# Performance work log

Measured on AMD Instinct MI355X. Metric: run time of the kernel, lower is better.

## Reference

```python
import jax, jax.numpy as jnp
import numpy as np
import math

B, T, EMB = 2, 2048, 2048
HQ = HKV = 16
HD = EMB // HQ  # 128
MAX_SEQ = 2048


def _rope(x, cos, sin):
    # x: [b, t, h, d]; pairs are consecutive (view_as_complex on reshape(..., -1, 2))
    b, t, h, d = x.shape
    xp = x.astype(jnp.float32).reshape(b, t, h, d // 2, 2)
    xr, xi = xp[..., 0], xp[..., 1]
    c = cos[None, :, None, :]  # [1, t, 1, d/2]
    s = sin[None, :, None, :]
    or_ = xr * c - xi * s
    oi_ = xr * s + xi * c
    out = jnp.stack([or_, oi_], axis=-1).reshape(b, t, h, d)
    return out.astype(x.dtype)


def setup_inputs() -> dict:
    key = jax.random.key(0)
    ks = jax.random.split(key, 6)
    x = jax.random.normal(ks[0], (B, T, EMB), dtype=jnp.float32)
    # torch Linear weights: [out_features, in_features], y = x @ W.T
    sc = 1.0 / math.sqrt(EMB)
    wq = jax.random.normal(ks[1], (EMB, EMB), dtype=jnp.float32) * sc
    wk = jax.random.normal(ks[2], (EMB, EMB), dtype=jnp.float32) * sc
    wv = jax.random.normal(ks[3], (EMB, EMB), dtype=jnp.float32) * sc
    wo = jax.random.normal(ks[4], (EMB, EMB), dtype=jnp.float32) * sc
    # RoPE frequencies (llama-style), head_dim/2 angles per position
    inv_freq = 1.0 / (10000.0 ** (np.arange(0, HD, 2, dtype=np.float32) / HD))
    angles = np.arange(T, dtype=np.float32)[:, None] * inv_freq[None, :]  # [T, HD/2]
    freqs_cos = jnp.asarray(np.cos(angles))
    freqs_sin = jnp.asarray(np.sin(angles))
    k_cache = jnp.zeros((B, MAX_SEQ, HKV, HD), dtype=jnp.float32)
    v_cache = jnp.zeros((B, MAX_SEQ, HKV, HD), dtype=jnp.float32)
    return {"x": x, "wq": wq, "wk": wk, "wv": wv, "wo": wo,
            "k_cache": k_cache, "v_cache": v_cache,
            "freqs_cos": freqs_cos, "freqs_sin": freqs_sin, "start_pos": 0}


def reference(x, wq, wk, wv, wo, k_cache, v_cache, freqs_cos, freqs_sin, start_pos):
    b, t, c = x.shape
    xq = (x @ wq.T).reshape(b, t, HQ, HD)
    xk = (x @ wk.T).reshape(b, t, HKV, HD)
    xv = (x @ wv.T).reshape(b, t, HKV, HD)
    xq = _rope(xq, freqs_cos, freqs_sin)
    xk = _rope(xk, freqs_cos, freqs_sin)
    # KV-cache update at start_pos, then read prefix [0, start_pos+t)
    k_cache = jax.lax.dynamic_update_slice(k_cache, xk, (0, start_pos, 0, 0))
    v_cache = jax.lax.dynamic_update_slice(v_cache, xv, (0, start_pos, 0, 0))
    keys = k_cache[:, :start_pos + t]    # [b, s, hkv, d]
    values = v_cache[:, :start_pos + t]
    # n_rep = HQ // HKV = 1 -> repeat_kv is identity
    q = xq.transpose(0, 2, 1, 3)         # [b, h, t, d]
    k = keys.transpose(0, 2, 1, 3)       # [b, h, s, d]
    v = values.transpose(0, 2, 1, 3)
    scores = jnp.einsum('bhtd,bhsd->bhts', q, k) / math.sqrt(HD)
    scores = jax.nn.softmax(scores.astype(jnp.float32), axis=-1).astype(q.dtype)
    out = jnp.einsum('bhts,bhsd->bhtd', scores, v)
    out = out.transpose(0, 2, 1, 3).reshape(b, t, -1)
    return out @ wo.T
```

## Files before the change

kernel.cpp:

```cpp
#include <hip/hip_runtime.h>
#include <cstdint>

using u16 = unsigned short;
using short8 = __attribute__((ext_vector_type(8))) short;
using floatx4 = __attribute__((ext_vector_type(4))) float;

__device__ __forceinline__ u16 f2b(float f) {
    unsigned u = __float_as_uint(f);
    u = (u + 0x7fffu + ((u >> 16) & 1u)) >> 16;
    return (u16)u;
}
__device__ __forceinline__ u16 f2b_fast(float f) {
    return (u16)((__float_as_uint(f) + 0x8000u) >> 16);
}
__device__ __forceinline__ float b2f(unsigned v) {
    return __uint_as_float(v << 16);
}
__device__ __forceinline__ float fast_exp2(float f) {
#if __has_builtin(__builtin_amdgcn_exp2f)
    return __builtin_amdgcn_exp2f(f);
#else
    return exp2f(f);
#endif
}
__device__ __forceinline__ void gl_lds16(const u16* g, u16* l) {
    __builtin_amdgcn_global_load_lds(
        (const __attribute__((address_space(1))) void*)(const void*)g,
        (__attribute__((address_space(3))) void*)(void*)l, 16, 0, 0);
}

__global__ void cvt5_kernel(const float* __restrict__ x, const float* __restrict__ wq,
                            const float* __restrict__ wk, const float* __restrict__ wv,
                            const float* __restrict__ wo, u16* __restrict__ xb,
                            u16* __restrict__ wqkvb, u16* __restrict__ wob) {
    int i = blockIdx.x * 256 + threadIdx.x;
    const float* src;
    u16* dst;
    int off;
    if (i < 2097152)      { src = x;  dst = xb;             off = i; }
    else if (i < 3145728) { src = wq; dst = wqkvb;          off = i - 2097152; }
    else if (i < 4194304) { src = wk; dst = wqkvb + 4194304; off = i - 3145728; }
    else if (i < 5242880) { src = wv; dst = wqkvb + 8388608; off = i - 4194304; }
    else                  { src = wo; dst = wob;            off = i - 5242880; }
    float4 v = ((const float4*)src)[off];
    uint2 o;
    o.x = (unsigned)f2b(v.x) | ((unsigned)f2b(v.y) << 16);
    o.y = (unsigned)f2b(v.z) | ((unsigned)f2b(v.w) << 16);
    *(uint2*)&dst[off * 4] = o;
}

template <int OUT_F32, int DO_ROPE>
__global__ void gemm_bt(const u16* __restrict__ A, const u16* __restrict__ B,
                        void* __restrict__ Cp, const float* __restrict__ fc,
                        const float* __restrict__ fs, int M, int N, int K) {
    __shared__ u16 As[128 * 64];
    __shared__ u16 Bs[128 * 64];
    const int tid = threadIdx.x;
    const int lane = tid & 63, w = tid >> 6;
    const int wm = w & 1, wn = w >> 1;
    const int m0 = blockIdx.y * 128, n0 = blockIdx.x * 128;
    const int r = lane & 15, q = lane >> 4;

    floatx4 acc[4][4] = {};

    for (int k0 = 0; k0 < K; k0 += 64) {
        __syncthreads();
#pragma unroll
        for (int i = 0; i < 4; i++) {
            int c = i * 256 + tid;
            int row = c >> 3, slot = c & 7;
            int sch = (slot ^ (row & 7)) * 8;
            gl_lds16(A + (size_t)(m0 + row) * K + k0 + sch, As + c * 8);
            gl_lds16(B + (size_t)(n0 + row) * K + k0 + sch, Bs + c * 8);
        }
        __syncthreads();
#pragma unroll
        for (int ks = 0; ks < 2; ks++) {
            const int sw = ((ks * 4 + q) ^ (r & 7)) * 8;
            short8 af[4], bf[4];
#pragma unroll
            for (int mi = 0; mi < 4; mi++)
                af[mi] = *(const short8*)&As[(wm * 64 + mi * 16 + r) * 64 + sw];
#pragma unroll
            for (int ni = 0; ni < 4; ni++)
                bf[ni] = *(const short8*)&Bs[(wn * 64 + ni * 16 + r) * 64 + sw];
#pragma unroll
            for (int mi = 0; mi < 4; mi++)
#pragma unroll
                for (int ni = 0; ni < 4; ni++)
                    acc[mi][ni] = __builtin_amdgcn_mfma_f32_16x16x32_bf16(af[mi], bf[ni], acc[mi][ni], 0, 0, 0);
        }
    }
    const bool rope = DO_ROPE && (n0 < 4096);
#pragma unroll
    for (int mi = 0; mi < 4; mi++)
#pragma unroll
        for (int ni = 0; ni < 4; ni++)
#pragma unroll
            for (int rr = 0; rr < 4; rr++) {
                int row = m0 + wm * 64 + mi * 16 + q * 4 + rr;
                int col = n0 + wn * 64 + ni * 16 + r;
                float val = acc[mi][ni][rr];
                if (rope) {
                    int t = row & 2047;
                    int d2 = (col & 127) >> 1;
                    float cv = fc[t * 64 + d2], sv = fs[t * 64 + d2];
                    float partner = __shfl_xor(val, 1);
                    val = (r & 1) ? (partner * sv + val * cv)
                                  : (val * cv - partner * sv);
                }
                if (OUT_F32)
                    ((float*)Cp)[(size_t)row * N + col] = val;
                else
                    ((u16*)Cp)[(size_t)row * N + col] = f2b(val);
            }
}

__global__ void vtrans_kernel(const u16* __restrict__ xqkv, u16* __restrict__ vt) {
    __shared__ u16 Ts[64][72];
    int bh = blockIdx.z, d0 = blockIdx.y * 64, t0 = blockIdx.x * 64;
    int b = bh >> 4, h = bh & 15;
#pragma unroll
    for (int i = 0; i < 2; i++) {
        int c = i * 256 + threadIdx.x;
        int tr = c >> 3, c8 = (c & 7) * 8;
        short8 v = *(const short8*)&xqkv[(size_t)(b * 2048 + t0 + tr) * 6144 + 4096 + h * 128 + d0 + c8];
#pragma unroll
        for (int j = 0; j < 8; j++) Ts[tr][c8 + j] = ((u16)v[j]);
    }
    __syncthreads();
#pragma unroll
    for (int i = 0; i < 2; i++) {
        int c = i * 256 + threadIdx.x;
        int dr = c >> 3, t8 = (c & 7) * 8;
        short8 v;
#pragma unroll
        for (int j = 0; j < 8; j++) v[j] = (short)Ts[t8 + j][dr];
        *(short8*)&vt[((size_t)(bh * 128 + d0 + dr)) * 2048 + t0 + t8] = v;
    }
}

__global__ __launch_bounds__(256, 2) void flash_kernel(const u16* __restrict__ xqkv,
                                                       const u16* __restrict__ vt,
                                                       u16* __restrict__ ao) {
    __shared__ u16 smem[25600];
    u16* Ks = smem;
    u16* Vs = smem + 8192;
    const int tid = threadIdx.x;
    const int lane = tid & 63, w = tid >> 6;
    const int qg = lane >> 4, r16 = lane & 15;
    const int swz = (qg ^ ((r16 >> 1) & 3)) * 8;
    u16* QPw = smem + 16384 + w * 2304;
    const int bh = blockIdx.y, b = bh >> 4, h = bh & 15;
    const int t0 = blockIdx.x * 128 + w * 32;
    const float sl2e = 0.08838834764831845f * 1.4426950408889634f;

    short8 qreg[2][4];
#pragma unroll
    for (int tf = 0; tf < 2; tf++)
#pragma unroll
        for (int kc = 0; kc < 4; kc++) {
            short8 qv = *(const short8*)&xqkv[(size_t)(b * 2048 + t0 + tf * 16 + r16) * 6144 +
                                              h * 128 + kc * 32 + qg * 8];
#pragma unroll
            for (int j = 0; j < 8; j++)
                qv[j] = (short)f2b(b2f((u16)qv[j]) * sl2e);
            qreg[tf][kc] = qv;
        }

    floatx4 oacc[2][8] = {};
    float lsum[2][4] = {};

    for (int s0 = 0; s0 < 2048; s0 += 64) {
        __syncthreads();
#pragma unroll
        for (int i = 0; i < 4; i++) {
            int c = i * 256 + tid;
            int kc = c >> 8, cc = c & 255, sr = cc >> 2, slot = cc & 3;
            int sch = (slot ^ ((sr >> 1) & 3)) * 8;
            gl_lds16(xqkv + (size_t)(b * 2048 + s0 + sr) * 6144 + 2048 + h * 128 + kc * 32 + sch,
                     Ks + c * 8);
        }
#pragma unroll
        for (int i = 0; i < 4; i++) {
            int c = i * 256 + tid;
            int sc = c >> 9, cc = c & 511, d = cc >> 2, slot = cc & 3;
            int sch = (slot ^ ((d >> 1) & 3)) * 8;
            gl_lds16(vt + (size_t)(bh * 128 + d) * 2048 + s0 + sc * 32 + sch, Vs + c * 8);
        }
        __syncthreads();

        floatx4 sacc[2][4] = {};
#pragma unroll
        for (int kc = 0; kc < 4; kc++)
#pragma unroll
            for (int ni = 0; ni < 4; ni++) {
                short8 bfr = *(const short8*)&Ks[kc * 2048 + (ni * 16 + r16) * 32 + swz];
                sacc[0][ni] = __builtin_amdgcn_mfma_f32_16x16x32_bf16(qreg[0][kc], bfr, sacc[0][ni], 0, 0, 0);
                sacc[1][ni] = __builtin_amdgcn_mfma_f32_16x16x32_bf16(qreg[1][kc], bfr, sacc[1][ni], 0, 0, 0);
            }

#pragma unroll
        for (int tf = 0; tf < 2; tf++)
#pragma unroll
            for (int ni = 0; ni < 4; ni++)
#pragma unroll
                for (int r = 0; r < 4; r++) {
                    float p = fast_exp2(sacc[tf][ni][r]);
                    lsum[tf][r] += p;
                    QPw[(tf * 16 + qg * 4 + r) * 72 + ni * 16 + r16] = f2b_fast(p);
                }

#pragma unroll
        for (int sc = 0; sc < 2; sc++) {
            short8 p0 = *(const short8*)&QPw[(r16) * 72 + sc * 32 + qg * 8];
            short8 p1 = *(const short8*)&QPw[(16 + r16) * 72 + sc * 32 + qg * 8];
#pragma unroll
            for (int dt = 0; dt < 8; dt++) {
                short8 a = *(const short8*)&Vs[sc * 4096 + (dt * 16 + r16) * 32 + swz];
                oacc[0][dt] = __builtin_amdgcn_mfma_f32_16x16x32_bf16(a, p0, oacc[0][dt], 0, 0, 0);
                oacc[1][dt] = __builtin_amdgcn_mfma_f32_16x16x32_bf16(a, p1, oacc[1][dt], 0, 0, 0);
            }
        }
    }

#pragma unroll
    for (int mm = 1; mm <= 8; mm <<= 1)
#pragma unroll
        for (int tf = 0; tf < 2; tf++)
#pragma unroll
            for (int r = 0; r < 4; r++) lsum[tf][r] += __shfl_xor(lsum[tf][r], mm);

    int src = (r16 >> 2) << 4;
#pragma unroll
    for (int tf = 0; tf < 2; tf++) {
        float l0 = __shfl(lsum[tf][0], src), l1 = __shfl(lsum[tf][1], src);
        float l2 = __shfl(lsum[tf][2], src), l3 = __shfl(lsum[tf][3], src);
        float lsel = (r16 & 2) ? ((r16 & 1) ? l3 : l2) : ((r16 & 1) ? l1 : l0);
        float inv = 1.0f / lsel;
#pragma unroll
        for (int dt = 0; dt < 8; dt++)
#pragma unroll
            for (int r = 0; r < 4; r++)
                QPw[r16 * 136 + dt * 16 + qg * 4 + r] = f2b(oacc[tf][dt][r] * inv);
#pragma unroll
        for (int i = 0; i < 4; i++) {
            int c = i * 64 + lane;
            int rowt = c >> 4, c8 = (c & 15) * 8;
            short8 v = *(const short8*)&QPw[rowt * 136 + c8];
            *(short8*)&ao[(size_t)(b * 2048 + t0 + tf * 16 + rowt) * 2048 + h * 128 + c8] = v;
        }
    }
}

extern "C" void kernel_launch(void* const* d_in, const int* in_sizes, int n_in,
                              void* d_out, int out_size, void* d_ws, size_t ws_size,
                              hipStream_t stream) {
    const float* x = (const float*)d_in[0];
    const float* wq = (const float*)d_in[1];
    const float* wk = (const float*)d_in[2];
    const float* wv = (const float*)d_in[3];
    const float* wo = (const float*)d_in[4];
    const float* fcos = (const float*)d_in[7];
    const float* fsin = (const float*)d_in[8];

    char* ws = (char*)d_ws;
    u16* xb    = (u16*)(ws);
    u16* wqkvb = (u16*)(ws + 16777216);
    u16* wob   = (u16*)(ws + 41943040);
    u16* xqkv  = (u16*)(ws + 50331648);
    u16* vt    = (u16*)(ws + 100663296);
    u16* ao    = (u16*)(ws + 117440512);

    cvt5_kernel<<<24576, 256, 0, stream>>>(x, wq, wk, wv, wo, xb, wqkvb, wob);
    gemm_bt<0, 1><<<dim3(48, 32), 256, 0, stream>>>(xb, wqkvb, xqkv, fcos, fsin, 4096, 6144, 2048);
    vtrans_kernel<<<dim3(32, 2, 32), 256, 0, stream>>>(xqkv, vt);
    flash_kernel<<<dim3(16, 32), 256, 0, stream>>>(xqkv, vt, ao);
    gemm_bt<1, 0><<<dim3(16, 32), 256, 0, stream>>>(ao, wob, (float*)d_out, nullptr, nullptr, 4096, 2048, 2048);
}
```

Baseline: 443.6 us.

## Replace QKV projection GEMM with 256x256 tiled, double-buffered, ping-pong MFMA kernel

Adds a new gemm256 kernel for the fused QKV projection. It uses 256x256 tiles with 512 threads, asynchronous global-to-LDS loads double-buffered across K tiles, swizzled LDS reads and 16x16x32 bf16 MFMA with setprio to interleave memory and compute. The goal is more operand reuse per load and better latency hiding than the 128x128 gemm_bt. RoPE stays fused in the epilogue. The cost is high register pressure, 64KB of LDS per block, and only 384 blocks, which may leave some CUs unevenly loaded.

```diff
diff --git a/kernel.cpp b/kernel.cpp
--- a/kernel.cpp
+++ b/kernel.cpp
@@ -28,6 +28,13 @@
         (const __attribute__((address_space(1))) void*)(const void*)g,
         (__attribute__((address_space(3))) void*)(void*)l, 16, 0, 0);
 }
+
+#define BARF()                                  \
+    do {                                        \
+        asm volatile("" ::: "memory");          \
+        __builtin_amdgcn_s_barrier();           \
+        asm volatile("" ::: "memory");          \
+    } while (0)
 
 __global__ void cvt5_kernel(const float* __restrict__ x, const float* __restrict__ wq,
                             const float* __restrict__ wk, const float* __restrict__ wv,
@@ -49,6 +56,119 @@
     *(uint2*)&dst[off * 4] = o;
 }
 
+#define MFMA16(MH)                                                             \
+    __builtin_amdgcn_s_setprio(1);                                             \
+    _Pragma("unroll") for (int i_ = 0; i_ < 4; i_++) {                         \
+        _Pragma("unroll") for (int n_ = 0; n_ < 4; n_++)                       \
+            acc[(MH) * 4 + i_][n_] = __builtin_amdgcn_mfma_f32_16x16x32_bf16(  \
+                af[i_], bf[n_], acc[(MH) * 4 + i_][n_], 0, 0, 0);              \
+    }                                                                          \
+    __builtin_amdgcn_s_setprio(0);
+
+template <int DO_ROPE>
+__global__ __launch_bounds__(512, 2) void gemm256(const u16* __restrict__ A,
+                                                  const u16* __restrict__ B,
+                                                  u16* __restrict__ C,
+                                                  const float* __restrict__ fc,
+                                                  const float* __restrict__ fs,
+                                                  int M, int N, int K) {
+    __shared__ u16 lds[2][2][2][8192];
+    const int tid = threadIdx.x;
+    const int lane = tid & 63, w = tid >> 6;
+    const int wm = w >> 2, wn = w & 3;
+    const int m0 = blockIdx.y * 256, n0 = blockIdx.x * 256;
+    const int r16 = lane & 15, qg = lane >> 4;
+    const int swz8 = (qg ^ ((r16 >> 1) & 3)) * 8;
+    const int nt = K >> 6;
+
+    const int sr = tid >> 2;
+    const int sc0 = ((tid & 3) ^ ((sr >> 1) & 3)) * 8;
+    const size_t offA0 = (size_t)(m0 + sr) * K + sc0;
+    const size_t offB0 = (size_t)(n0 + sr) * K + sc0;
+    const size_t off1 = (size_t)128 * K;
+
+    auto stage = [&](int mat, int ks, int tile) {
+        const u16* s = (mat ? B + offB0 : A + offA0) + tile * 64 + ks * 32;
+        u16* d = &lds[tile & 1][mat][ks][tid * 8];
+        gl_lds16(s, d);
+        gl_lds16(s + off1, d + 4096);
+    };
+
+    floatx4 acc[8][4] = {};
+
+    stage(0, 0, 0); stage(1, 0, 0); stage(0, 1, 0); stage(1, 1, 0);
+    stage(0, 0, 1); stage(1, 0, 1); stage(0, 1, 1);
+    asm volatile("s_waitcnt vmcnt(6)" ::: "memory");
+    BARF();
+
+    const int abase = (wm * 128 + r16) * 32 + swz8;
+    const int bbase = (wn * 64 + r16) * 32 + swz8;
+
+    for (int t = 0; t < nt; ++t) {
+        const int buf = t & 1;
+        const u16* LA0 = &lds[buf][0][0][0];
+        const u16* LA1 = &lds[buf][0][1][0];
+        const u16* LB0 = &lds[buf][1][0][0];
+        const u16* LB1 = &lds[buf][1][1][0];
+        short8 af[4], bf[4];
+
+#pragma unroll
+        for (int n_ = 0; n_ < 4; n_++) bf[n_] = *(const short8*)&LB0[bbase + n_ * 512];
+#pragma unroll
+        for (int i_ = 0; i_ < 4; i_++) af[i_] = *(const short8*)&LA0[abase + i_ * 512];
+        if (t + 1 < nt) stage(1, 1, t + 1);
+        BARF();
+        MFMA16(0)
+        BARF();
+
+#pragma unroll
+        for (int i_ = 0; i_ < 4; i_++) af[i_] = *(const short8*)&LA0[abase + 2048 + i_ * 512];
+        BARF();
+        MFMA16(1)
+        if (t + 2 < nt) stage(0, 0, t + 2);
+        BARF();
+
+#pragma unroll
+        for (int n_ = 0; n_ < 4; n_++) bf[n_] = *(const short8*)&LB1[bbase + n_ * 512];
+#pragma unroll
+        for (int i_ = 0; i_ < 4; i_++) af[i_] = *(const short8*)&LA1[abase + i_ * 512];
+        if (t + 2 < nt) stage(1, 0, t + 2);
+        BARF();
+        MFMA16(0)
+        BARF();
+
+#pragma unroll
+        for (int i_ = 0; i_ < 4; i_++) af[i_] = *(const short8*)&LA1[abase + 2048 + i_ * 512];
+        BARF();
+        MFMA16(1)
+        if (t + 2 < nt) stage(0, 1, t + 2);
+        if (t + 2 < nt)      asm volatile("s_waitcnt vmcnt(6)" ::: "memory");
+        else if (t + 1 < nt) asm volatile("s_waitcnt vmcnt(0)" ::: "memory");
+        BARF();
+    }
+
+    const bool rope = DO_ROPE && (n0 < 4096);
+#pragma unroll
+    for (int mi = 0; mi < 8; mi++)
+#pragma unroll
+        for (int ni = 0; ni < 4; ni++)
+#pragma unroll
+            for (int rr = 0; rr < 4; rr++) {
+                int row = m0 + wm * 128 + mi * 16 + qg * 4 + rr;
+                int col = n0 + wn * 64 + ni * 16 + r16;
+                float val = acc[mi][ni][rr];
+                if (rope) {
+                    int tt = row & 2047;
+                    int d2 = (col & 127) >> 1;
+                    float cv = fc[tt * 64 + d2], sv = fs[tt * 64 + d2];
+                    float partner = __shfl_xor(val, 1);
+                    val = (r16 & 1) ? (partner * sv + val * cv)
+                                    : (val * cv - partner * sv);
+                }
+                C[(size_t)row * N + col] = f2b(val);
+            }
+}
+
 template <int OUT_F32, int DO_ROPE>
 __global__ void gemm_bt(const u16* __restrict__ A, const u16* __restrict__ B,
                         void* __restrict__ Cp, const float* __restrict__ fc,
@@ -273,7 +393,7 @@
     u16* ao    = (u16*)(ws + 117440512);
 
     cvt5_kernel<<<24576, 256, 0, stream>>>(x, wq, wk, wv, wo, xb, wqkvb, wob);
-    gemm_bt<0, 1><<<dim3(48, 32), 256, 0, stream>>>(xb, wqkvb, xqkv, fcos, fsin, 4096, 6144, 2048);
+    gemm256<1><<<dim3(24, 16), 512, 0, stream>>>(xb, wqkvb, xqkv, fcos, fsin, 4096, 6144, 2048);
     vtrans_kernel<<<dim3(32, 2, 32), 256, 0, stream>>>(xqkv, vt);
     flash_kernel<<<dim3(16, 32), 256, 0, stream>>>(xqkv, vt, ao);
     gemm_bt<1, 0><<<dim3(16, 32), 256, 0, stream>>>(ao, wob, (float*)d_out, nullptr, nullptr, 4096, 2048, 2048);
```

Result: slower. 476.0 us (+7.3%).

## Read K/V fragments directly from global memory in flash kernel, drop LDS staging

Applied to the files above, without the earlier changes.

The flash attention kernel no longer stages K and V tiles into shared memory with barriers. Each wave now loads its MFMA B/A fragments straight from global memory, relying on L2/cache reuse across the four waves and across blocks. The grid is swapped so consecutive blocks share the same head, which improves cache locality for K/V. This removes the per-tile syncthreads and LDS traffic but turns each fragment read into a strided global load with higher latency and four-fold redundant traffic per block.

```diff
diff --git a/kernel.cpp b/kernel.cpp
--- a/kernel.cpp
+++ b/kernel.cpp
@@ -143,16 +143,13 @@
 __global__ __launch_bounds__(256, 2) void flash_kernel(const u16* __restrict__ xqkv,
                                                        const u16* __restrict__ vt,
                                                        u16* __restrict__ ao) {
-    __shared__ u16 smem[25600];
-    u16* Ks = smem;
-    u16* Vs = smem + 8192;
+    __shared__ u16 QP[4 * 2304];
     const int tid = threadIdx.x;
     const int lane = tid & 63, w = tid >> 6;
     const int qg = lane >> 4, r16 = lane & 15;
-    const int swz = (qg ^ ((r16 >> 1) & 3)) * 8;
-    u16* QPw = smem + 16384 + w * 2304;
-    const int bh = blockIdx.y, b = bh >> 4, h = bh & 15;
-    const int t0 = blockIdx.x * 128 + w * 32;
+    u16* QPw = QP + w * 2304;
+    const int bh = blockIdx.x, b = bh >> 4, h = bh & 15;
+    const int t0 = blockIdx.y * 128 + w * 32;
     const float sl2e = 0.08838834764831845f * 1.4426950408889634f;
 
     short8 qreg[2][4];
@@ -171,31 +168,19 @@
     floatx4 oacc[2][8] = {};
     float lsum[2][4] = {};
 
+    const u16* Kg0 = xqkv + (size_t)(b * 2048) * 6144 + 2048 + h * 128;
+    const u16* Vg0 = vt + (size_t)(bh * 128) * 2048;
+
     for (int s0 = 0; s0 < 2048; s0 += 64) {
-        __syncthreads();
-#pragma unroll
-        for (int i = 0; i < 4; i++) {
-            int c = i * 256 + tid;
-            int kc = c >> 8, cc = c & 255, sr = cc >> 2, slot = cc & 3;
-            int sch = (slot ^ ((sr >> 1) & 3)) * 8;
-            gl_lds16(xqkv + (size_t)(b * 2048 + s0 + sr) * 6144 + 2048 + h * 128 + kc * 32 + sch,
-                     Ks + c * 8);
-        }
-#pragma unroll
-        for (int i = 0; i < 4; i++) {
-            int c = i * 256 + tid;
-            int sc = c >> 9, cc = c & 511, d = cc >> 2, slot = cc & 3;
-            int sch = (slot ^ ((d >> 1) & 3)) * 8;
-            gl_lds16(vt + (size_t)(bh * 128 + d) * 2048 + s0 + sc * 32 + sch, Vs + c * 8);
-        }
-        __syncthreads();
+        const u16* Kg = Kg0 + (size_t)s0 * 6144;
+        const u16* Vg = Vg0 + s0;
 
         floatx4 sacc[2][4] = {};
 #pragma unroll
         for (int kc = 0; kc < 4; kc++)
 #pragma unroll
             for (int ni = 0; ni < 4; ni++) {
-                short8 bfr = *(const short8*)&Ks[kc * 2048 + (ni * 16 + r16) * 32 + swz];
+                short8 bfr = *(const short8*)&Kg[(size_t)(ni * 16 + r16) * 6144 + kc * 32 + qg * 8];
                 sacc[0][ni] = __builtin_amdgcn_mfma_f32_16x16x32_bf16(qreg[0][kc], bfr, sacc[0][ni], 0, 0, 0);
                 sacc[1][ni] = __builtin_amdgcn_mfma_f32_16x16x32_bf16(qreg[1][kc], bfr, sacc[1][ni], 0, 0, 0);
             }
@@ -217,7 +202,7 @@
             short8 p1 = *(const short8*)&QPw[(16 + r16) * 72 + sc * 32 + qg * 8];
 #pragma unroll
             for (int dt = 0; dt < 8; dt++) {
-                short8 a = *(const short8*)&Vs[sc * 4096 + (dt * 16 + r16) * 32 + swz];
+                short8 a = *(const short8*)&Vg[(size_t)(dt * 16 + r16) * 2048 + sc * 32 + qg * 8];
                 oacc[0][dt] = __builtin_amdgcn_mfma_f32_16x16x32_bf16(a, p0, oacc[0][dt], 0, 0, 0);
                 oacc[1][dt] = __builtin_amdgcn_mfma_f32_16x16x32_bf16(a, p1, oacc[1][dt], 0, 0, 0);
             }
@@ -275,6 +260,6 @@
     cvt5_kernel<<<24576, 256, 0, stream>>>(x, wq, wk, wv, wo, xb, wqkvb, wob);
     gemm_bt<0, 1><<<dim3(48, 32), 256, 0, stream>>>(xb, wqkvb, xqkv, fcos, fsin, 4096, 6144, 2048);
     vtrans_kernel<<<dim3(32, 2, 32), 256, 0, stream>>>(xqkv, vt);
-    flash_kernel<<<dim3(16, 32), 256, 0, stream>>>(xqkv, vt, ao);
+    flash_kernel<<<dim3(32, 16), 256, 0, stream>>>(xqkv, vt, ao);
     gemm_bt<1, 0><<<dim3(16, 32), 256, 0, stream>>>(ao, wob, (float*)d_out, nullptr, nullptr, 4096, 2048, 2048);
 }
```

Measured after the change: 557.7 us. 25.7% more time.

## Double-buffer K tiles and split V load wait in flash attention

Applied to the files above, without the earlier changes.

Restructures the flash attention loop so the next K tile is prefetched into a second LDS buffer while the current tile is processed. The V tile load is issued at the start of each iteration and waited on only before the PV MFMAs, using explicit vmcnt waits and raw s_barrier with scheduling barriers. It also swaps the grid dimensions so blocks for the same batch-head are launched adjacently, which may change L2 reuse of K/V. The change costs 16 KB more LDS per block, which could affect occupancy, and depends on hand-counted vmcnt values being correct.

```diff
diff --git a/kernel.cpp b/kernel.cpp
--- a/kernel.cpp
+++ b/kernel.cpp
@@ -28,6 +28,18 @@
         (const __attribute__((address_space(1))) void*)(const void*)g,
         (__attribute__((address_space(3))) void*)(void*)l, 16, 0, 0);
 }
+
+#define ABAR()                                   \
+    do {                                         \
+        __builtin_amdgcn_sched_barrier(0);       \
+        asm volatile("s_barrier");               \
+        __builtin_amdgcn_sched_barrier(0);       \
+    } while (0)
+#define VMCNT(n)                                      \
+    do {                                              \
+        asm volatile("s_waitcnt vmcnt(" #n ")");      \
+        __builtin_amdgcn_sched_barrier(0);            \
+    } while (0)
 
 __global__ void cvt5_kernel(const float* __restrict__ x, const float* __restrict__ wq,
                             const float* __restrict__ wk, const float* __restrict__ wv,
@@ -143,44 +155,28 @@
 __global__ __launch_bounds__(256, 2) void flash_kernel(const u16* __restrict__ xqkv,
                                                        const u16* __restrict__ vt,
                                                        u16* __restrict__ ao) {
-    __shared__ u16 smem[25600];
-    u16* Ks = smem;
-    u16* Vs = smem + 8192;
+    __shared__ u16 smem[33792];
+    u16* Vs = smem + 16384;
     const int tid = threadIdx.x;
     const int lane = tid & 63, w = tid >> 6;
     const int qg = lane >> 4, r16 = lane & 15;
     const int swz = (qg ^ ((r16 >> 1) & 3)) * 8;
-    u16* QPw = smem + 16384 + w * 2304;
-    const int bh = blockIdx.y, b = bh >> 4, h = bh & 15;
-    const int t0 = blockIdx.x * 128 + w * 32;
+    u16* QPw = smem + 24576 + w * 2304;
+    const int bh = blockIdx.x, b = bh >> 4, h = bh & 15;
+    const int t0 = blockIdx.y * 128 + w * 32;
     const float sl2e = 0.08838834764831845f * 1.4426950408889634f;
 
-    short8 qreg[2][4];
-#pragma unroll
-    for (int tf = 0; tf < 2; tf++)
-#pragma unroll
-        for (int kc = 0; kc < 4; kc++) {
-            short8 qv = *(const short8*)&xqkv[(size_t)(b * 2048 + t0 + tf * 16 + r16) * 6144 +
-                                              h * 128 + kc * 32 + qg * 8];
-#pragma unroll
-            for (int j = 0; j < 8; j++)
-                qv[j] = (short)f2b(b2f((u16)qv[j]) * sl2e);
-            qreg[tf][kc] = qv;
-        }
-
-    floatx4 oacc[2][8] = {};
-    float lsum[2][4] = {};
-
-    for (int s0 = 0; s0 < 2048; s0 += 64) {
-        __syncthreads();
+    auto stageK = [&](int s0, int kb) {
 #pragma unroll
         for (int i = 0; i < 4; i++) {
             int c = i * 256 + tid;
             int kc = c >> 8, cc = c & 255, sr = cc >> 2, slot = cc & 3;
             int sch = (slot ^ ((sr >> 1) & 3)) * 8;
             gl_lds16(xqkv + (size_t)(b * 2048 + s0 + sr) * 6144 + 2048 + h * 128 + kc * 32 + sch,
-                     Ks + c * 8);
-        }
+                     smem + kb * 8192 + c * 8);
+        }
+    };
+    auto stageV = [&](int s0) {
 #pragma unroll
         for (int i = 0; i < 4; i++) {
             int c = i * 256 + tid;
@@ -188,8 +184,34 @@
             int sch = (slot ^ ((d >> 1) & 3)) * 8;
             gl_lds16(vt + (size_t)(bh * 128 + d) * 2048 + s0 + sc * 32 + sch, Vs + c * 8);
         }
-        __syncthreads();
-
+    };
+
+    short8 qreg[2][4];
+#pragma unroll
+    for (int tf = 0; tf < 2; tf++)
+#pragma unroll
+        for (int kc = 0; kc < 4; kc++) {
+            short8 qv = *(const short8*)&xqkv[(size_t)(b * 2048 + t0 + tf * 16 + r16) * 6144 +
+                                              h * 128 + kc * 32 + qg * 8];
+#pragma unroll
+            for (int j = 0; j < 8; j++)
+                qv[j] = (short)f2b(b2f((u16)qv[j]) * sl2e);
+            qreg[tf][kc] = qv;
+        }
+
+    floatx4 oacc[2][8] = {};
+    float lsum[2][4] = {};
+
+    stageK(0, 0);
+    int kb = 0;
+
+    for (int s0 = 0; s0 < 2048; s0 += 64) {
+        stageV(s0);
+        stageK((s0 + 64) & 2047, kb ^ 1);
+        VMCNT(8);
+        ABAR();
+
+        const u16* Ks = smem + kb * 8192;
         floatx4 sacc[2][4] = {};
 #pragma unroll
         for (int kc = 0; kc < 4; kc++)
@@ -211,6 +233,9 @@
                     QPw[(tf * 16 + qg * 4 + r) * 72 + ni * 16 + r16] = f2b_fast(p);
                 }
 
+        VMCNT(4);
+        ABAR();
+
 #pragma unroll
         for (int sc = 0; sc < 2; sc++) {
             short8 p0 = *(const short8*)&QPw[(r16) * 72 + sc * 32 + qg * 8];
@@ -222,6 +247,9 @@
                 oacc[1][dt] = __builtin_amdgcn_mfma_f32_16x16x32_bf16(a, p1, oacc[1][dt], 0, 0, 0);
             }
         }
+
+        ABAR();
+        kb ^= 1;
     }
 
 #pragma unroll
@@ -275,6 +303,6 @@
     cvt5_kernel<<<24576, 256, 0, stream>>>(x, wq, wk, wv, wo, xb, wqkvb, wob);
     gemm_bt<0, 1><<<dim3(48, 32), 256, 0, stream>>>(xb, wqkvb, xqkv, fcos, fsin, 4096, 6144, 2048);
     vtrans_kernel<<<dim3(32, 2, 32), 256, 0, stream>>>(xqkv, vt);
-    flash_kernel<<<dim3(16, 32), 256, 0, stream>>>(xqkv, vt, ao);
+    flash_kernel<<<dim3(32, 16), 256, 0, stream>>>(xqkv, vt, ao);
     gemm_bt<1, 0><<<dim3(16, 32), 256, 0, stream>>>(ao, wob, (float*)d_out, nullptr, nullptr, 4096, 2048, 2048);
 }
```

Measured after the change: 419.2 us. -5.5%, faster.
